# Kernel optimization log

Hardware: AMD Instinct MI355X
Metric: run time of the kernel (lower is better)

## Reference

```python
import jax, jax.numpy as jnp
import numpy as np

OUT, IN, G = 12288, 4096, 128
TOKENS = 8192


def setup_inputs() -> dict:
    key = jax.random.key(0)
    k1, k2, k3, k4 = jax.random.split(key, 4)
    hidden_states = (jax.random.normal(k1, (TOKENS, IN), dtype=jnp.float32) * 0.05).astype(jnp.float16)
    # packed uint8 byte stored as int32: low nibble -> row 2k, high nibble -> row 2k+1
    weight = jax.random.randint(k2, (OUT // 2, IN), 0, 256, dtype=jnp.int32)
    weight_scale = (jax.random.uniform(k3, (OUT, IN // G), dtype=jnp.float32) * 0.02 + 1e-3).astype(jnp.float16)
    pre_quant_scale = (jax.random.uniform(k4, (IN,), dtype=jnp.float32) + 0.5).astype(jnp.float16)
    return {
        'hidden_states': hidden_states,
        'weight': weight,
        'weight_scale': weight_scale,
        'pre_quant_scale': pre_quant_scale,
    }


def _dequantize(weight, weight_scale):
    # unpack two signed int4 values per byte along the output dim
    low = (weight & 0xF) - 8           # [OUT//2, IN]
    high = ((weight >> 4) & 0xF) - 8   # [OUT//2, IN]
    w_int = jnp.stack([low, high], axis=1).reshape(OUT, IN).astype(jnp.float16)
    scales = jnp.repeat(weight_scale, G, axis=1)  # [OUT, IN], per-group fp16 scale
    return w_int * scales


def reference(hidden_states, weight, weight_scale, pre_quant_scale):
    x = hidden_states * pre_quant_scale          # pre-quant activation scaling (fp16)
    W = _dequantize(weight, weight_scale)        # [OUT, IN] fp16
    return jnp.einsum('ti,oi->to', x, W)         # [TOKENS, OUT]
```

## Files before the change

### kernel.cpp

```cpp
#include <hip/hip_runtime.h>

#define TOKENS  8192
#define IN_DIM  4096
#define OUT_DIM 12288
#define GRP     128

typedef __attribute__((ext_vector_type(8))) short  short8;
typedef __attribute__((ext_vector_type(8))) unsigned short ushort8;
typedef __attribute__((ext_vector_type(4))) float  f32x4;

#define BARRIER() asm volatile("s_barrier" ::: "memory")

__device__ __forceinline__ unsigned short f2bf(float f) {
    union { float f; unsigned int i; } x; x.f = f;
    unsigned int r = x.i + 0x7FFFu + ((x.i >> 16) & 1u);
    return (unsigned short)(r >> 16);
}

__device__ __forceinline__ void gload_lds16(const void* g, void* l) {
    __builtin_amdgcn_global_load_lds(
        (const __attribute__((address_space(1))) void*)g,
        (__attribute__((address_space(3))) void*)l, 16, 0, 0);
}

#define DQ_BLOCKS 24576
#define CV_BLOCKS 16384

__global__ void prep_kernel(const int* __restrict__ wp,
                            const float* __restrict__ wsc,
                            const float* __restrict__ pqs,
                            const float* __restrict__ hid,
                            unsigned short* __restrict__ Wd,
                            unsigned short* __restrict__ Abf) {
    if (blockIdx.x < DQ_BLOCKS) {
        int idx = blockIdx.x * blockDim.x + threadIdx.x;
        int p  = idx >> 10;
        int i0 = (idx & 1023) << 2;
        int g  = i0 >> 7;
        const int4 w = *reinterpret_cast<const int4*>(wp + (size_t)p * IN_DIM + i0);
        float slo = wsc[(size_t)(2 * p)     * (IN_DIM / GRP) + g];
        float shi = wsc[(size_t)(2 * p + 1) * (IN_DIM / GRP) + g];
        float4 q = *reinterpret_cast<const float4*>(pqs + i0);
        float qf[4] = { q.x, q.y, q.z, q.w };
        int   wv[4] = { w.x, w.y, w.z, w.w };
        ushort4 lo, hi;
        unsigned short* lop = (unsigned short*)&lo;
        unsigned short* hig = (unsigned short*)&hi;
#pragma unroll
        for (int j = 0; j < 4; ++j) {
            lop[j] = f2bf((float)(( wv[j]       & 0xF) - 8) * slo * qf[j]);
            hig[j] = f2bf((float)(((wv[j] >> 4) & 0xF) - 8) * shi * qf[j]);
        }
        *reinterpret_cast<ushort4*>(Wd + (size_t)(2 * p)     * IN_DIM + i0) = lo;
        *reinterpret_cast<ushort4*>(Wd + (size_t)(2 * p + 1) * IN_DIM + i0) = hi;
    } else {
        size_t base = ((size_t)(blockIdx.x - DQ_BLOCKS) * blockDim.x + threadIdx.x) * 8;
        float4 a = *reinterpret_cast<const float4*>(hid + base);
        float4 b = *reinterpret_cast<const float4*>(hid + base + 4);
        ushort8 v;
        v[0] = f2bf(a.x); v[1] = f2bf(a.y); v[2] = f2bf(a.z); v[3] = f2bf(a.w);
        v[4] = f2bf(b.x); v[5] = f2bf(b.y); v[6] = f2bf(b.z); v[7] = f2bf(b.w);
        *reinterpret_cast<ushort8*>(Abf + base) = v;
    }
}

#define BM 256
#define BN 256
#define BK 64
#define NT (IN_DIM / BK)

__device__ __forceinline__ void stage_chunk(const unsigned short* gbase, int rowbase,
                                            int t, int kh, char* region, int tid) {
#pragma unroll
    for (int c = 0; c < 2; ++c) {
        int off  = c * 8192 + tid * 16;
        int row  = off >> 6;
        int slot = (off >> 4) & 3;
        int col  = t * 64 + kh * 32 + ((slot ^ ((row >> 1) & 3)) << 3);
        gload_lds16(gbase + (size_t)(rowbase + row) * IN_DIM + col, region + off);
    }
}

__global__ __launch_bounds__(512, 2) void gemm8p_kernel(
    const unsigned short* __restrict__ A,
    const unsigned short* __restrict__ B,
    float* __restrict__ C) {

    __shared__ char lds[2][2][2][16384];

    const int tid  = threadIdx.x;
    const int lane = tid & 63;
    const int wid  = tid >> 6;
    const int wm   = wid >> 2;
    const int wn   = wid & 3;
    const int lq   = lane & 15;
    const int lr   = lane >> 4;
    const int sw   = (lr ^ ((lq >> 1) & 3)) << 4;

    int bid = blockIdx.x;
    int swz = (bid & 7) * 192 + (bid >> 3);
    const int brow = (swz / (OUT_DIM / BN)) * BM;
    const int bcol = (swz % (OUT_DIM / BN)) * BN;

    f32x4 acc[8][4] = {};
    short8 aE[4], A1[4], bE[4], B1[4];

    stage_chunk(A, brow, 0, 0, &lds[0][0][0][0], tid);
    stage_chunk(B, bcol, 0, 0, &lds[0][1][0][0], tid);
    stage_chunk(A, brow, 0, 1, &lds[0][0][1][0], tid);
    stage_chunk(B, bcol, 0, 1, &lds[0][1][1][0], tid);
    stage_chunk(A, brow, 1, 0, &lds[1][0][0][0], tid);
    stage_chunk(B, bcol, 1, 0, &lds[1][1][0][0], tid);
    asm volatile("s_waitcnt vmcnt(8)" ::: "memory");
    BARRIER();
#pragma unroll
    for (int m = 0; m < 4; ++m)
        aE[m] = *reinterpret_cast<const short8*>(
            &lds[0][0][0][(wm * 128 + m * 16 + lq) * 64 + sw]);
#pragma unroll
    for (int n = 0; n < 4; ++n)
        bE[n] = *reinterpret_cast<const short8*>(
            &lds[0][1][0][(wn * 64 + n * 16 + lq) * 64 + sw]);

    for (int t = 0; t < NT; ++t) {
        const int p = t & 1, q = p ^ 1;

#pragma unroll
        for (int m = 0; m < 4; ++m)
            A1[m] = *reinterpret_cast<const short8*>(
                &lds[p][0][0][(wm * 128 + (m + 4) * 16 + lq) * 64 + sw]);
        if (t + 1 < NT) stage_chunk(A, brow, t + 1, 1, &lds[q][0][1][0], tid);
#pragma unroll
        for (int m = 0; m < 4; ++m)
#pragma unroll
            for (int n = 0; n < 4; ++n)
                acc[m][n] = __builtin_amdgcn_mfma_f32_16x16x32_bf16(
                    aE[m], bE[n], acc[m][n], 0, 0, 0);
        if (t + 1 < NT) { asm volatile("s_waitcnt vmcnt(6)" ::: "memory"); }
        else            { asm volatile("s_waitcnt vmcnt(0)" ::: "memory"); }
        BARRIER();

#pragma unroll
        for (int m = 0; m < 4; ++m)
            aE[m] = *reinterpret_cast<const short8*>(
                &lds[p][0][1][(wm * 128 + m * 16 + lq) * 64 + sw]);
#pragma unroll
        for (int n = 0; n < 4; ++n)
            B1[n] = *reinterpret_cast<const short8*>(
                &lds[p][1][1][(wn * 64 + n * 16 + lq) * 64 + sw]);
        if (t + 1 < NT) stage_chunk(B, bcol, t + 1, 1, &lds[q][1][1][0], tid);
#pragma unroll
        for (int m = 0; m < 4; ++m)
#pragma unroll
            for (int n = 0; n < 4; ++n)
                acc[m + 4][n] = __builtin_amdgcn_mfma_f32_16x16x32_bf16(
                    A1[m], bE[n], acc[m + 4][n], 0, 0, 0);
        BARRIER();

#pragma unroll
        for (int m = 0; m < 4; ++m)
            A1[m] = *reinterpret_cast<const short8*>(
                &lds[p][0][1][(wm * 128 + (m + 4) * 16 + lq) * 64 + sw]);
        if (t + 2 < NT) stage_chunk(A, brow, t + 2, 0, &lds[p][0][0][0], tid);
#pragma unroll
        for (int m = 0; m < 4; ++m)
#pragma unroll
            for (int n = 0; n < 4; ++n)
                acc[m][n] = __builtin_amdgcn_mfma_f32_16x16x32_bf16(
                    aE[m], B1[n], acc[m][n], 0, 0, 0);
        if (t + 1 < NT) {
            if (t + 2 < NT) { asm volatile("s_waitcnt vmcnt(6)" ::: "memory"); }
            else            { asm volatile("s_waitcnt vmcnt(4)" ::: "memory"); }
        }
        BARRIER();

        if (t + 1 < NT) {
#pragma unroll
            for (int m = 0; m < 4; ++m)
                aE[m] = *reinterpret_cast<const short8*>(
                    &lds[q][0][0][(wm * 128 + m * 16 + lq) * 64 + sw]);
#pragma unroll
            for (int n = 0; n < 4; ++n)
                bE[n] = *reinterpret_cast<const short8*>(
                    &lds[q][1][0][(wn * 64 + n * 16 + lq) * 64 + sw]);
        }
        if (t + 2 < NT) stage_chunk(B, bcol, t + 2, 0, &lds[p][1][0][0], tid);
#pragma unroll
        for (int m = 0; m < 4; ++m)
#pragma unroll
            for (int n = 0; n < 4; ++n)
                acc[m + 4][n] = __builtin_amdgcn_mfma_f32_16x16x32_bf16(
                    A1[m], B1[n], acc[m + 4][n], 0, 0, 0);
        BARRIER();
    }

#pragma unroll
    for (int m = 0; m < 8; ++m)
#pragma unroll
        for (int n = 0; n < 4; ++n)
#pragma unroll
            for (int j = 0; j < 4; ++j) {
                int row = brow + wm * 128 + m * 16 + lr * 4 + j;
                int col = bcol + wn * 64 + n * 16 + lq;
                C[(size_t)row * OUT_DIM + col] = acc[m][n][j];
            }
}

template <bool CONV_A, bool FUSED_B>
__global__ __launch_bounds__(256) void gemm_fb_kernel(
    const void* __restrict__ Ap, const unsigned short* __restrict__ Bd,
    const int* __restrict__ Wp, const float* __restrict__ wsc,
    const float* __restrict__ pqs, float* __restrict__ C) {
    __shared__ short sA[128 * 64];
    __shared__ short sB[128 * 64];
    const int tid  = threadIdx.x;
    const int lane = tid & 63;
    const int w    = tid >> 6;
    const int wr   = w >> 1, wc = w & 1;
    const int lr   = lane >> 4;
    const int lq   = lane & 15;
    const int nbn = OUT_DIM / 128;
    int bid = blockIdx.x;
    int swzb = (bid & 7) * ((TOKENS / 128) * nbn / 8) + (bid >> 3);
    const int brow = (swzb / nbn) * 128;
    const int bcol = (swzb % nbn) * 128;
    f32x4 acc[4][4] = {};
    for (int k0 = 0; k0 < IN_DIM; k0 += 64) {
#pragma unroll
        for (int c = 0; c < 4; ++c) {
            int off  = c * 4096 + tid * 16;
            int r    = off >> 7;
            if constexpr (CONV_A) {
                int e = (off & 127) >> 1;
                const float* src = (const float*)Ap + (size_t)(brow + r) * IN_DIM + k0 + e;
                float4 f0 = *reinterpret_cast<const float4*>(src);
                float4 f1 = *reinterpret_cast<const float4*>(src + 4);
                ushort8 v;
                v[0] = f2bf(f0.x); v[1] = f2bf(f0.y); v[2] = f2bf(f0.z); v[3] = f2bf(f0.w);
                v[4] = f2bf(f1.x); v[5] = f2bf(f1.y); v[6] = f2bf(f1.z); v[7] = f2bf(f1.w);
                *reinterpret_cast<ushort8*>((char*)sA + off) = v;
            } else {
                int colb = off & 127;
                gload_lds16((const char*)Ap + ((size_t)(brow + r) * IN_DIM + k0) * 2 + colb,
                            (char*)sA + off);
            }
            if constexpr (!FUSED_B) {
                int colb = off & 127;
                gload_lds16((const char*)Bd + ((size_t)(bcol + r) * IN_DIM + k0) * 2 + colb,
                            (char*)sB + off);
            }
        }
        if constexpr (FUSED_B) {
#pragma unroll
            for (int c = 0; c < 4; ++c) {
                int pr = c * 16 + (tid >> 4);
                int i0 = (tid & 15) * 4;
                int gp = (bcol >> 1) + pr;
                int gk = k0 + i0;
                int4 wv = *reinterpret_cast<const int4*>(Wp + (size_t)gp * IN_DIM + gk);
                int g = gk >> 7;
                float slo = wsc[(size_t)(2 * gp)     * (IN_DIM / GRP) + g];
                float shi = wsc[(size_t)(2 * gp + 1) * (IN_DIM / GRP) + g];
                float4 qv = *reinterpret_cast<const float4*>(pqs + gk);
                float qf[4] = { qv.x, qv.y, qv.z, qv.w };
                int wi[4] = { wv.x, wv.y, wv.z, wv.w };
                ushort4 lo, hi;
                unsigned short* lop = (unsigned short*)&lo;
                unsigned short* hig = (unsigned short*)&hi;
#pragma unroll
                for (int j = 0; j < 4; ++j) {
                    lop[j] = f2bf((float)(( wi[j]       & 0xF) - 8) * slo * qf[j]);
                    hig[j] = f2bf((float)(((wi[j] >> 4) & 0xF) - 8) * shi * qf[j]);
                }
                *reinterpret_cast<ushort4*>(&sB[(2 * pr)     * 64 + i0]) = lo;
                *reinterpret_cast<ushort4*>(&sB[(2 * pr + 1) * 64 + i0]) = hi;
            }
        }
        __syncthreads();
#pragma unroll
        for (int kk = 0; kk < 64; kk += 32) {
            int ko = kk + lr * 8;
            short8 af[4], bf[4];
#pragma unroll
            for (int m = 0; m < 4; ++m)
                af[m] = *reinterpret_cast<const short8*>(&sA[(wr * 64 + m * 16 + lq) * 64 + ko]);
#pragma unroll
            for (int n = 0; n < 4; ++n)
                bf[n] = *reinterpret_cast<const short8*>(&sB[(wc * 64 + n * 16 + lq) * 64 + ko]);
#pragma unroll
            for (int m = 0; m < 4; ++m)
#pragma unroll
                for (int n = 0; n < 4; ++n)
                    acc[m][n] = __builtin_amdgcn_mfma_f32_16x16x32_bf16(
                        af[m], bf[n], acc[m][n], 0, 0, 0);
        }
        __syncthreads();
    }
#pragma unroll
    for (int m = 0; m < 4; ++m)
#pragma unroll
        for (int n = 0; n < 4; ++n)
#pragma unroll
            for (int j = 0; j < 4; ++j) {
                int row = brow + wr * 64 + m * 16 + lr * 4 + j;
                int col = bcol + wc * 64 + n * 16 + lq;
                C[(size_t)row * OUT_DIM + col] = acc[m][n][j];
            }
}

extern "C" void kernel_launch(void* const* d_in, const int* in_sizes, int n_in,
                              void* d_out, int out_size, void* d_ws, size_t ws_size,
                              hipStream_t stream) {
    const void* p_hidden = nullptr; const void* p_weight = nullptr;
    const void* p_wscale = nullptr; const void* p_pqs = nullptr;
    for (int i = 0; i < n_in; ++i) {
        switch (in_sizes[i]) {
            case 33554432: p_hidden = d_in[i]; break;
            case 25165824: p_weight = d_in[i]; break;
            case 393216:   p_wscale = d_in[i]; break;
            case 4096:     p_pqs    = d_in[i]; break;
            default: break;
        }
    }
    if (!p_hidden || !p_weight || !p_wscale || !p_pqs) {
        p_hidden = d_in[0]; p_weight = d_in[1]; p_wscale = d_in[2]; p_pqs = d_in[3];
    }
    const float* hidden = (const float*)p_hidden;
    const int*   weight = (const int*)p_weight;
    const float* wscale = (const float*)p_wscale;
    const float* pqs    = (const float*)p_pqs;
    float*       out    = (float*)d_out;

    const size_t wd_bytes = (size_t)OUT_DIM * IN_DIM * 2;
    const size_t ab_bytes = (size_t)TOKENS * IN_DIM * 2;

    if (ws_size >= wd_bytes + ab_bytes) {
        unsigned short* Wd  = (unsigned short*)d_ws;
        unsigned short* Abf = (unsigned short*)((char*)d_ws + wd_bytes);
        prep_kernel<<<DQ_BLOCKS + CV_BLOCKS, 256, 0, stream>>>(
            weight, wscale, pqs, hidden, Wd, Abf);
        gemm8p_kernel<<<(TOKENS / BM) * (OUT_DIM / BN), 512, 0, stream>>>(Abf, Wd, out);
    } else if (ws_size >= wd_bytes) {
        unsigned short* Wd = (unsigned short*)d_ws;
        prep_kernel<<<DQ_BLOCKS, 256, 0, stream>>>(
            weight, wscale, pqs, hidden, Wd, nullptr);
        gemm_fb_kernel<true, false><<<(TOKENS / 128) * (OUT_DIM / 128), 256, 0, stream>>>(
            hidden, Wd, nullptr, nullptr, nullptr, out);
    } else {
        gemm_fb_kernel<true, true><<<(TOKENS / 128) * (OUT_DIM / 128), 256, 0, stream>>>(
            hidden, nullptr, weight, wscale, pqs, out);
    }
}
```

Baseline: 795.3 us.

## Restructure 256x256 GEMM main loop into four-quadrant schedule with per-wave group staging

The bf16 GEMM main loop is rewritten. Each iteration now loads full-K (64) A and B fragments for a quadrant of the warp tile and runs four MFMA phases, one per 128x... sub-quadrant, with s_setprio raised around the MFMA bursts. Global-to-LDS staging is changed so each wave loads rows belonging to its own row group rather than a flat chunk split. The prefetch schedule is reorganised (B one tile ahead, A two ahead) to overlap memory with compute. The price is more barriers per iteration and different register pressure, and the new wait counts must match the issue order exactly.

```diff
diff --git a/kernel.cpp b/kernel.cpp
--- a/kernel.cpp
+++ b/kernel.cpp
@@ -10,6 +10,7 @@
 typedef __attribute__((ext_vector_type(4))) float  f32x4;
 
 #define BARRIER() asm volatile("s_barrier" ::: "memory")
+#define LGKM0()   asm volatile("s_waitcnt lgkmcnt(0)" ::: "memory")
 
 __device__ __forceinline__ unsigned short f2bf(float f) {
     union { float f; unsigned int i; } x; x.f = f;
@@ -69,15 +70,18 @@
 #define BK 64
 #define NT (IN_DIM / BK)
 
-__device__ __forceinline__ void stage_chunk(const unsigned short* gbase, int rowbase,
-                                            int t, int kh, char* region, int tid) {
-#pragma unroll
-    for (int c = 0; c < 2; ++c) {
-        int off  = c * 8192 + tid * 16;
-        int row  = off >> 6;
+__device__ __forceinline__ void stage_group(const unsigned short* gbase,
+                                            int blockbase, int growbase,
+                                            int t, char* mat_base, int gti) {
+#pragma unroll
+    for (int c = 0; c < 4; ++c) {
+        int kh   = c >> 1;
+        int off  = (c & 1) * 4096 + gti * 16;
+        int row  = growbase + (off >> 6);
         int slot = (off >> 4) & 3;
         int col  = t * 64 + kh * 32 + ((slot ^ ((row >> 1) & 3)) << 3);
-        gload_lds16(gbase + (size_t)(rowbase + row) * IN_DIM + col, region + off);
+        gload_lds16(gbase + (size_t)(blockbase + row) * IN_DIM + col,
+                    mat_base + kh * 16384 + row * 64 + (slot << 4));
     }
 }
 
@@ -93,9 +97,13 @@
     const int wid  = tid >> 6;
     const int wm   = wid >> 2;
     const int wn   = wid & 3;
+    const int bg   = wn >> 1;
     const int lq   = lane & 15;
     const int lr   = lane >> 4;
     const int sw   = (lr ^ ((lq >> 1) & 3)) << 4;
+
+    const int gtiA = (wn) * 64 + lane;
+    const int gtiB = (((wid >> 2) << 1) | (wid & 1)) * 64 + lane;
 
     int bid = blockIdx.x;
     int swz = (bid & 7) * 192 + (bid >> 3);
@@ -103,94 +111,102 @@
     const int bcol = (swz % (OUT_DIM / BN)) * BN;
 
     f32x4 acc[8][4] = {};
-    short8 aE[4], A1[4], bE[4], B1[4];
-
-    stage_chunk(A, brow, 0, 0, &lds[0][0][0][0], tid);
-    stage_chunk(B, bcol, 0, 0, &lds[0][1][0][0], tid);
-    stage_chunk(A, brow, 0, 1, &lds[0][0][1][0], tid);
-    stage_chunk(B, bcol, 0, 1, &lds[0][1][1][0], tid);
-    stage_chunk(A, brow, 1, 0, &lds[1][0][0][0], tid);
-    stage_chunk(B, bcol, 1, 0, &lds[1][1][0][0], tid);
-    asm volatile("s_waitcnt vmcnt(8)" ::: "memory");
+    short8 aF[4][2], bF0[2][2], bF1[2][2];
+
+    stage_group(A, brow, wm * 128, 0, &lds[0][0][0][0], gtiA);
+    stage_group(B, bcol, bg * 128, 0, &lds[0][1][0][0], gtiB);
+    stage_group(A, brow, wm * 128, 1, &lds[1][0][0][0], gtiA);
+    asm volatile("s_waitcnt vmcnt(4)" ::: "memory");
     BARRIER();
-#pragma unroll
-    for (int m = 0; m < 4; ++m)
-        aE[m] = *reinterpret_cast<const short8*>(
-            &lds[0][0][0][(wm * 128 + m * 16 + lq) * 64 + sw]);
-#pragma unroll
-    for (int n = 0; n < 4; ++n)
-        bE[n] = *reinterpret_cast<const short8*>(
-            &lds[0][1][0][(wn * 64 + n * 16 + lq) * 64 + sw]);
-
-    for (int t = 0; t < NT; ++t) {
-        const int p = t & 1, q = p ^ 1;
-
-#pragma unroll
-        for (int m = 0; m < 4; ++m)
-            A1[m] = *reinterpret_cast<const short8*>(
-                &lds[p][0][0][(wm * 128 + (m + 4) * 16 + lq) * 64 + sw]);
-        if (t + 1 < NT) stage_chunk(A, brow, t + 1, 1, &lds[q][0][1][0], tid);
-#pragma unroll
-        for (int m = 0; m < 4; ++m)
-#pragma unroll
-            for (int n = 0; n < 4; ++n)
-                acc[m][n] = __builtin_amdgcn_mfma_f32_16x16x32_bf16(
-                    aE[m], bE[n], acc[m][n], 0, 0, 0);
-        if (t + 1 < NT) { asm volatile("s_waitcnt vmcnt(6)" ::: "memory"); }
+
+    for (int u = 0; u < NT; ++u) {
+        const int p = u & 1, q = p ^ 1;
+        char* pA = &lds[p][0][0][0];
+        char* pB = &lds[p][1][0][0];
+
+#pragma unroll
+        for (int m = 0; m < 4; ++m)
+#pragma unroll
+            for (int kk = 0; kk < 2; ++kk)
+                aF[m][kk] = *reinterpret_cast<const short8*>(
+                    pA + kk * 16384 + (wm * 128 + m * 16 + lq) * 64 + sw);
+#pragma unroll
+        for (int n = 0; n < 2; ++n)
+#pragma unroll
+            for (int kk = 0; kk < 2; ++kk)
+                bF0[n][kk] = *reinterpret_cast<const short8*>(
+                    pB + kk * 16384 + (wn * 64 + n * 16 + lq) * 64 + sw);
+        if (u + 1 < NT)
+            stage_group(B, bcol, bg * 128, u + 1, &lds[q][1][0][0], gtiB);
+        BARRIER();
+        LGKM0();
+        __builtin_amdgcn_s_setprio(1);
+#pragma unroll
+        for (int m = 0; m < 4; ++m)
+#pragma unroll
+            for (int n = 0; n < 2; ++n)
+#pragma unroll
+                for (int kk = 0; kk < 2; ++kk)
+                    acc[m][n] = __builtin_amdgcn_mfma_f32_16x16x32_bf16(
+                        aF[m][kk], bF0[n][kk], acc[m][n], 0, 0, 0);
+        __builtin_amdgcn_s_setprio(0);
+        BARRIER();
+
+#pragma unroll
+        for (int n = 0; n < 2; ++n)
+#pragma unroll
+            for (int kk = 0; kk < 2; ++kk)
+                bF1[n][kk] = *reinterpret_cast<const short8*>(
+                    pB + kk * 16384 + (wn * 64 + 32 + n * 16 + lq) * 64 + sw);
+        BARRIER();
+        LGKM0();
+        __builtin_amdgcn_s_setprio(1);
+#pragma unroll
+        for (int m = 0; m < 4; ++m)
+#pragma unroll
+            for (int n = 0; n < 2; ++n)
+#pragma unroll
+                for (int kk = 0; kk < 2; ++kk)
+                    acc[m][n + 2] = __builtin_amdgcn_mfma_f32_16x16x32_bf16(
+                        aF[m][kk], bF1[n][kk], acc[m][n + 2], 0, 0, 0);
+        __builtin_amdgcn_s_setprio(0);
+        BARRIER();
+
+#pragma unroll
+        for (int m = 0; m < 4; ++m)
+#pragma unroll
+            for (int kk = 0; kk < 2; ++kk)
+                aF[m][kk] = *reinterpret_cast<const short8*>(
+                    pA + kk * 16384 + (wm * 128 + 64 + m * 16 + lq) * 64 + sw);
+        BARRIER();
+        LGKM0();
+        __builtin_amdgcn_s_setprio(1);
+#pragma unroll
+        for (int m = 0; m < 4; ++m)
+#pragma unroll
+            for (int n = 0; n < 2; ++n)
+#pragma unroll
+                for (int kk = 0; kk < 2; ++kk)
+                    acc[m + 4][n] = __builtin_amdgcn_mfma_f32_16x16x32_bf16(
+                        aF[m][kk], bF0[n][kk], acc[m + 4][n], 0, 0, 0);
+        __builtin_amdgcn_s_setprio(0);
+        BARRIER();
+
+        if (u + 2 < NT)
+            stage_group(A, brow, wm * 128, u + 2, &lds[p][0][0][0], gtiA);
+        BARRIER();
+        __builtin_amdgcn_s_setprio(1);
+#pragma unroll
+        for (int m = 0; m < 4; ++m)
+#pragma unroll
+            for (int n = 0; n < 2; ++n)
+#pragma unroll
+                for (int kk = 0; kk < 2; ++kk)
+                    acc[m + 4][n + 2] = __builtin_amdgcn_mfma_f32_16x16x32_bf16(
+                        aF[m][kk], bF1[n][kk], acc[m + 4][n + 2], 0, 0, 0);
+        __builtin_amdgcn_s_setprio(0);
+        if (u + 2 < NT) { asm volatile("s_waitcnt vmcnt(4)" ::: "memory"); }
         else            { asm volatile("s_waitcnt vmcnt(0)" ::: "memory"); }
-        BARRIER();
-
-#pragma unroll
-        for (int m = 0; m < 4; ++m)
-            aE[m] = *reinterpret_cast<const short8*>(
-                &lds[p][0][1][(wm * 128 + m * 16 + lq) * 64 + sw]);
-#pragma unroll
-        for (int n = 0; n < 4; ++n)
-            B1[n] = *reinterpret_cast<const short8*>(
-                &lds[p][1][1][(wn * 64 + n * 16 + lq) * 64 + sw]);
-        if (t + 1 < NT) stage_chunk(B, bcol, t + 1, 1, &lds[q][1][1][0], tid);
-#pragma unroll
-        for (int m = 0; m < 4; ++m)
-#pragma unroll
-            for (int n = 0; n < 4; ++n)
-                acc[m + 4][n] = __builtin_amdgcn_mfma_f32_16x16x32_bf16(
-                    A1[m], bE[n], acc[m + 4][n], 0, 0, 0);
-        BARRIER();
-
-#pragma unroll
-        for (int m = 0; m < 4; ++m)
-            A1[m] = *reinterpret_cast<const short8*>(
-                &lds[p][0][1][(wm * 128 + (m + 4) * 16 + lq) * 64 + sw]);
-        if (t + 2 < NT) stage_chunk(A, brow, t + 2, 0, &lds[p][0][0][0], tid);
-#pragma unroll
-        for (int m = 0; m < 4; ++m)
-#pragma unroll
-            for (int n = 0; n < 4; ++n)
-                acc[m][n] = __builtin_amdgcn_mfma_f32_16x16x32_bf16(
-                    aE[m], B1[n], acc[m][n], 0, 0, 0);
-        if (t + 1 < NT) {
-            if (t + 2 < NT) { asm volatile("s_waitcnt vmcnt(6)" ::: "memory"); }
-            else            { asm volatile("s_waitcnt vmcnt(4)" ::: "memory"); }
-        }
-        BARRIER();
-
-        if (t + 1 < NT) {
-#pragma unroll
-            for (int m = 0; m < 4; ++m)
-                aE[m] = *reinterpret_cast<const short8*>(
-                    &lds[q][0][0][(wm * 128 + m * 16 + lq) * 64 + sw]);
-#pragma unroll
-            for (int n = 0; n < 4; ++n)
-                bE[n] = *reinterpret_cast<const short8*>(
-                    &lds[q][1][0][(wn * 64 + n * 16 + lq) * 64 + sw]);
-        }
-        if (t + 2 < NT) stage_chunk(B, bcol, t + 2, 0, &lds[p][1][0][0], tid);
-#pragma unroll
-        for (int m = 0; m < 4; ++m)
-#pragma unroll
-            for (int n = 0; n < 4; ++n)
-                acc[m + 4][n] = __builtin_amdgcn_mfma_f32_16x16x32_bf16(
-                    A1[m], B1[n], acc[m + 4][n], 0, 0, 0);
         BARRIER();
     }
 
```

Result: slower. 830.8 us (+4.5%).

## Load B operand directly from global into registers, bypassing LDS staging

Applied to the files above, without the earlier changes.

The B tile is no longer staged through shared memory. Each wave now reads its B fragments straight from global memory into registers, prefetching the next iteration's first half one step ahead. The explicit vmcnt waits for the A staging are removed, and the LDS footprint is halved. This avoids B's LDS write/read traffic and the associated barriers. In exchange it duplicates B global loads across the two wm waves, uses strided, less coalesced access, and exposes more global latency, since B1 is loaded in the same iteration it is used.

```diff
diff --git a/kernel.cpp b/kernel.cpp
--- a/kernel.cpp
+++ b/kernel.cpp
@@ -83,10 +83,10 @@
 
 __global__ __launch_bounds__(512, 2) void gemm8p_kernel(
     const unsigned short* __restrict__ A,
-    const unsigned short* __restrict__ B,
+    const unsigned short* __restrict__ Bp,
     float* __restrict__ C) {
 
-    __shared__ char lds[2][2][2][16384];
+    __shared__ char lds[2][2][16384];
 
     const int tid  = threadIdx.x;
     const int lane = tid & 63;
@@ -102,53 +102,50 @@
     const int brow = (swz / (OUT_DIM / BN)) * BM;
     const int bcol = (swz % (OUT_DIM / BN)) * BN;
 
+    const unsigned short* Bbase = Bp + (size_t)(bcol + wn * 64 + lq) * IN_DIM + lr * 8;
+
     f32x4 acc[8][4] = {};
-    short8 aE[4], A1[4], bE[4], B1[4];
-
-    stage_chunk(A, brow, 0, 0, &lds[0][0][0][0], tid);
-    stage_chunk(B, bcol, 0, 0, &lds[0][1][0][0], tid);
-    stage_chunk(A, brow, 0, 1, &lds[0][0][1][0], tid);
-    stage_chunk(B, bcol, 0, 1, &lds[0][1][1][0], tid);
-    stage_chunk(A, brow, 1, 0, &lds[1][0][0][0], tid);
-    stage_chunk(B, bcol, 1, 0, &lds[1][1][0][0], tid);
-    asm volatile("s_waitcnt vmcnt(8)" ::: "memory");
+    short8 aE[4], A1[4], bE[4], bN[4], B1[4];
+
+    stage_chunk(A, brow, 0, 0, &lds[0][0][0], tid);
+    stage_chunk(A, brow, 0, 1, &lds[0][1][0], tid);
+    stage_chunk(A, brow, 1, 0, &lds[1][0][0], tid);
+#pragma unroll
+    for (int n = 0; n < 4; ++n)
+        bN[n] = *reinterpret_cast<const short8*>(Bbase + (size_t)(n * 16) * IN_DIM + 0);
+    asm volatile("s_waitcnt vmcnt(4)" ::: "memory");
     BARRIER();
 #pragma unroll
     for (int m = 0; m < 4; ++m)
         aE[m] = *reinterpret_cast<const short8*>(
-            &lds[0][0][0][(wm * 128 + m * 16 + lq) * 64 + sw]);
-#pragma unroll
-    for (int n = 0; n < 4; ++n)
-        bE[n] = *reinterpret_cast<const short8*>(
-            &lds[0][1][0][(wn * 64 + n * 16 + lq) * 64 + sw]);
+            &lds[0][0][(wm * 128 + m * 16 + lq) * 64 + sw]);
 
     for (int t = 0; t < NT; ++t) {
         const int p = t & 1, q = p ^ 1;
 
 #pragma unroll
+        for (int n = 0; n < 4; ++n) bE[n] = bN[n];
+#pragma unroll
         for (int m = 0; m < 4; ++m)
             A1[m] = *reinterpret_cast<const short8*>(
-                &lds[p][0][0][(wm * 128 + (m + 4) * 16 + lq) * 64 + sw]);
-        if (t + 1 < NT) stage_chunk(A, brow, t + 1, 1, &lds[q][0][1][0], tid);
+                &lds[p][0][(wm * 128 + (m + 4) * 16 + lq) * 64 + sw]);
+#pragma unroll
+        for (int n = 0; n < 4; ++n)
+            B1[n] = *reinterpret_cast<const short8*>(
+                Bbase + (size_t)(n * 16) * IN_DIM + t * 64 + 32);
+        if (t + 1 < NT) stage_chunk(A, brow, t + 1, 1, &lds[q][1][0], tid);
 #pragma unroll
         for (int m = 0; m < 4; ++m)
 #pragma unroll
             for (int n = 0; n < 4; ++n)
                 acc[m][n] = __builtin_amdgcn_mfma_f32_16x16x32_bf16(
                     aE[m], bE[n], acc[m][n], 0, 0, 0);
-        if (t + 1 < NT) { asm volatile("s_waitcnt vmcnt(6)" ::: "memory"); }
-        else            { asm volatile("s_waitcnt vmcnt(0)" ::: "memory"); }
         BARRIER();
 
 #pragma unroll
         for (int m = 0; m < 4; ++m)
             aE[m] = *reinterpret_cast<const short8*>(
-                &lds[p][0][1][(wm * 128 + m * 16 + lq) * 64 + sw]);
-#pragma unroll
-        for (int n = 0; n < 4; ++n)
-            B1[n] = *reinterpret_cast<const short8*>(
-                &lds[p][1][1][(wn * 64 + n * 16 + lq) * 64 + sw]);
-        if (t + 1 < NT) stage_chunk(B, bcol, t + 1, 1, &lds[q][1][1][0], tid);
+                &lds[p][1][(wm * 128 + m * 16 + lq) * 64 + sw]);
 #pragma unroll
         for (int m = 0; m < 4; ++m)
 #pragma unroll
@@ -160,31 +157,28 @@
 #pragma unroll
         for (int m = 0; m < 4; ++m)
             A1[m] = *reinterpret_cast<const short8*>(
-                &lds[p][0][1][(wm * 128 + (m + 4) * 16 + lq) * 64 + sw]);
-        if (t + 2 < NT) stage_chunk(A, brow, t + 2, 0, &lds[p][0][0][0], tid);
+                &lds[p][1][(wm * 128 + (m + 4) * 16 + lq) * 64 + sw]);
+        if (t + 2 < NT) stage_chunk(A, brow, t + 2, 0, &lds[p][0][0], tid);
+        if (t + 1 < NT) {
+#pragma unroll
+            for (int n = 0; n < 4; ++n)
+                bN[n] = *reinterpret_cast<const short8*>(
+                    Bbase + (size_t)(n * 16) * IN_DIM + (t + 1) * 64);
+        }
 #pragma unroll
         for (int m = 0; m < 4; ++m)
 #pragma unroll
             for (int n = 0; n < 4; ++n)
                 acc[m][n] = __builtin_amdgcn_mfma_f32_16x16x32_bf16(
                     aE[m], B1[n], acc[m][n], 0, 0, 0);
-        if (t + 1 < NT) {
-            if (t + 2 < NT) { asm volatile("s_waitcnt vmcnt(6)" ::: "memory"); }
-            else            { asm volatile("s_waitcnt vmcnt(4)" ::: "memory"); }
-        }
         BARRIER();
 
         if (t + 1 < NT) {
 #pragma unroll
             for (int m = 0; m < 4; ++m)
                 aE[m] = *reinterpret_cast<const short8*>(
-                    &lds[q][0][0][(wm * 128 + m * 16 + lq) * 64 + sw]);
-#pragma unroll
-            for (int n = 0; n < 4; ++n)
-                bE[n] = *reinterpret_cast<const short8*>(
-                    &lds[q][1][0][(wn * 64 + n * 16 + lq) * 64 + sw]);
-        }
-        if (t + 2 < NT) stage_chunk(B, bcol, t + 2, 0, &lds[p][1][0][0], tid);
+                    &lds[q][0][(wm * 128 + m * 16 + lq) * 64 + sw]);
+        }
 #pragma unroll
         for (int m = 0; m < 4; ++m)
 #pragma unroll
```

New measurement: 1.043 ms. +31.2%, slower.
